# Performance work log

Hardware: AMD Instinct MI355X
Metric: run time of the kernel (lower is better)

## Reference

```python
import jax, jax.numpy as jnp
import numpy as np

N, E, FI, H, T, FO, B = 20000, 320000, 16, 100, 5, 20, 50
EPS = 1e-5


def _glorot(k, shape, fan_in):
    return jax.random.normal(k, shape, jnp.float32) / np.float32(np.sqrt(fan_in))


def setup_inputs():
    key = jax.random.key(0)
    ks = jax.random.split(key, 16)
    inp = {}
    inp['x'] = jax.random.normal(ks[0], (N, FI), jnp.float32)
    inp['edge_index'] = jax.random.randint(ks[1], (2, E), 0, N, jnp.int32)
    inp['edge_attr'] = jax.random.normal(ks[2], (E, 1), jnp.float32)
    inp['batch'] = jnp.sort(jax.random.randint(ks[3], (N,), 0, B, jnp.int32))
    # PNAConv layer 0: input_dim -> hidden (F_in=FI, F_out=FO per tower)
    inp['e0_w'] = _glorot(ks[4], (1, FI), 1); inp['e0_b'] = jnp.zeros((FI,), jnp.float32)
    inp['pre0_w'] = _glorot(ks[5], (T, 3 * FI, FI), 3 * FI); inp['pre0_b'] = jnp.zeros((T, FI), jnp.float32)
    inp['post0_w'] = _glorot(ks[6], (T, 17 * FI, FO), 17 * FI); inp['post0_b'] = jnp.zeros((T, FO), jnp.float32)
    inp['lin0_w'] = _glorot(ks[7], (H, H), H); inp['lin0_b'] = jnp.zeros((H,), jnp.float32)
    inp['bn0_g'] = jnp.ones((H,), jnp.float32); inp['bn0_b'] = jnp.zeros((H,), jnp.float32)
    # PNAConv layers 1..2 (hidden -> hidden), stacked on leading dim 2
    inp['eL_w'] = _glorot(ks[8], (2, 1, H), 1); inp['eL_b'] = jnp.zeros((2, H), jnp.float32)
    inp['preL_w'] = _glorot(ks[9], (2, T, 3 * H, H), 3 * H); inp['preL_b'] = jnp.zeros((2, T, H), jnp.float32)
    inp['postL_w'] = _glorot(ks[10], (2, T, 17 * H, FO), 17 * H); inp['postL_b'] = jnp.zeros((2, T, FO), jnp.float32)
    inp['linL_w'] = _glorot(ks[11], (2, H, H), H); inp['linL_b'] = jnp.zeros((2, H), jnp.float32)
    inp['bnL_g'] = jnp.ones((2, H), jnp.float32); inp['bnL_b'] = jnp.zeros((2, H), jnp.float32)
    # head MLP: H -> 50 -> 25 -> 1
    inp['mlp_w1'] = _glorot(ks[12], (H, 50), H); inp['mlp_b1'] = jnp.zeros((50,), jnp.float32)
    inp['mlp_w2'] = _glorot(ks[13], (50, 25), 50); inp['mlp_b2'] = jnp.zeros((25,), jnp.float32)
    inp['mlp_w3'] = _glorot(ks[14], (25, 1), 25); inp['mlp_b3'] = jnp.zeros((1,), jnp.float32)
    return inp


def _batch_norm(x, g, b):
    mu = x.mean(0)
    var = jnp.mean((x - mu) * (x - mu), 0)  # biased var, as BatchNorm1d (training)
    return (x - mu) * jax.lax.rsqrt(var + EPS) * g + b


def _pna_conv(x, src, dst, edge_attr, cnt, d, log_d, avg_log, avg_lin,
              ew, eb, pw, pb, qw, qb, lw, lb):
    # x: [N,f]; pw: [T,3f,f]; qw: [T,(1+16)f,FO]; lw: [H,H]
    n, f = x.shape
    t = pw.shape[0]
    e = edge_attr @ ew + eb  # [E,f] edge encoder (shared across towers)
    w_i, w_j, w_e = pw[:, :f], pw[:, f:2 * f], pw[:, 2 * f:]
    # pre-MLP on cat([x_i, x_j, e]) without materializing the concat
    m = (jnp.einsum('ef,tfg->etg', x[dst], w_i)
         + jnp.einsum('ef,tfg->etg', x[src], w_j)
         + jnp.einsum('ef,tfg->etg', e, w_e)
         + pb[None])  # [E,T,f]
    dn = d[:, None, None]
    msum = jax.ops.segment_sum(m, dst, n)
    mean = msum / dn
    mean_sq = jax.ops.segment_sum(m * m, dst, n) / dn
    std = jnp.sqrt(jax.nn.relu(mean_sq - mean * mean) + EPS)
    has = (cnt > 0)[:, None, None]
    mn = jnp.where(has, jax.ops.segment_min(m, dst, n), 0.0)
    mx = jnp.where(has, jax.ops.segment_max(m, dst, n), 0.0)
    agg = jnp.concatenate([mean, mn, mx, std], axis=-1)  # [N,T,4f]
    # degree scalers: identity, amplification, attenuation, linear
    scal = jnp.stack([jnp.ones_like(d), log_d / avg_log,
                      avg_log / log_d, d / avg_lin], 0)  # [4,N]
    w_x = qw[:, :f]  # [T,f,FO] block acting on skip features x
    w_s = qw[:, f:].reshape(t, 4, 4 * f, -1).transpose(1, 0, 2, 3)  # [4,T,4f,FO]
    h = (jnp.einsum('nf,tfg->ntg', x, w_x)
         + jnp.einsum('sn,ntf,stfg->ntg', scal, agg, w_s)
         + qb[None])  # [N,T,FO]
    return h.reshape(n, -1) @ lw + lb  # [N,H]


def _model(x, edge_attr, e0_w, e0_b, pre0_w, pre0_b, post0_w, post0_b,
           lin0_w, lin0_b, bn0_g, bn0_b, eL_w, eL_b, preL_w, preL_b,
           postL_w, postL_b, linL_w, linL_b, bnL_g, bnL_b,
           mlp_w1, mlp_b1, mlp_w2, mlp_b2, mlp_w3, mlp_b3,
           edge_index, batch):
    src, dst = edge_index[0], edge_index[1]
    cnt = jax.ops.segment_sum(jnp.ones((E,), x.dtype), dst, N)
    d = jnp.maximum(cnt, 1.0)
    log_d = jnp.log(d + 1.0)
    avg_lin = jnp.mean(cnt)                 # PNA avg_deg['lin']
    avg_log = jnp.mean(jnp.log(cnt + 1.0))  # PNA avg_deg['log']
    h = _pna_conv(x, src, dst, edge_attr, cnt, d, log_d, avg_log, avg_lin,
                  e0_w, e0_b, pre0_w, pre0_b, post0_w, post0_b, lin0_w, lin0_b)
    h = jax.nn.relu(_batch_norm(h, bn0_g, bn0_b))
    for i in range(2):  # zip(convs, batch_norms) -> only num_conv_layers blocks run
        h = _pna_conv(h, src, dst, edge_attr, cnt, d, log_d, avg_log, avg_lin,
                      eL_w[i], eL_b[i], preL_w[i], preL_b[i],
                      postL_w[i], postL_b[i], linL_w[i], linL_b[i])
        h = jax.nn.relu(_batch_norm(h, bnL_g[i], bnL_b[i]))
    # global mean pool over graphs
    gsum = jax.ops.segment_sum(h, batch, B)
    gcnt = jnp.maximum(jax.ops.segment_sum(jnp.ones((N,), h.dtype), batch, B), 1.0)
    g = gsum / gcnt[:, None]
    g = jax.nn.relu(g @ mlp_w1 + mlp_b1)
    g = jax.nn.relu(g @ mlp_w2 + mlp_b2)
    return g @ mlp_w3 + mlp_b3  # [B,1]


def reference(x, edge_attr, e0_w, e0_b, pre0_w, pre0_b, post0_w, post0_b,
              lin0_w, lin0_b, bn0_g, bn0_b, eL_w, eL_b, preL_w, preL_b,
              postL_w, postL_b, linL_w, linL_b, bnL_g, bnL_b,
              mlp_w1, mlp_b1, mlp_w2, mlp_b2, mlp_w3, mlp_b3,
              edge_index, batch):
    return _model(x, edge_attr, e0_w, e0_b, pre0_w, pre0_b, post0_w, post0_b,
                  lin0_w, lin0_b, bn0_g, bn0_b, eL_w, eL_b, preL_w, preL_b,
                  postL_w, postL_b, linL_w, linL_b, bnL_g, bnL_b,
                  mlp_w1, mlp_b1, mlp_w2, mlp_b2, mlp_w3, mlp_b3,
                  edge_index, batch)
```

## Files before the change

kernel.cpp:

```cpp
#include <hip/hip_runtime.h>
#include <hip/hip_bf16.h>
#include <cstddef>

#define N_  20000
#define E_  320000
#define FI_ 16
#define H_  100
#define T_  5
#define FO_ 20
#define B_  50
#define EPSF 1e-5f
#define PR_  200

typedef __attribute__((ext_vector_type(8))) short short8;
typedef __attribute__((ext_vector_type(4))) float f32x4;

static __device__ __forceinline__ unsigned short f2bf(float x) {
  unsigned int u = __builtin_bit_cast(unsigned int, x);
  unsigned int r = (u + 0x7FFFu + ((u >> 16) & 1u)) >> 16;
  return (unsigned short)r;
}
static __device__ __forceinline__ unsigned int packbf(float a, float b) {
  return (unsigned int)f2bf(a) | ((unsigned int)f2bf(b) << 16);
}
static __device__ __forceinline__ float bf2f_lo(unsigned int u) {
  return __builtin_bit_cast(float, (u & 0xFFFFu) << 16);
}
static __device__ __forceinline__ float bf2f_hi(unsigned int u) {
  return __builtin_bit_cast(float, u & 0xFFFF0000u);
}

__global__ void k_count(const int* __restrict__ dst, int* __restrict__ cnt) {
  int e = blockIdx.x * blockDim.x + threadIdx.x;
  if (e < E_) atomicAdd(&cnt[dst[e]], 1);
}

__global__ __launch_bounds__(1024) void k_scan(const int* __restrict__ cnt, int* __restrict__ rowptr) {
  __shared__ int ls[1024];
  const int tid = threadIdx.x;
  const int base = tid * 20;
  int loc[20];
  int lsum = 0;
  #pragma unroll
  for (int i = 0; i < 20; ++i) {
    int idx = base + i;
    int v = (idx < N_) ? cnt[idx] : 0;
    loc[i] = lsum;
    lsum += v;
  }
  ls[tid] = lsum;
  __syncthreads();
  for (int off = 1; off < 1024; off <<= 1) {
    int t = (tid >= off) ? ls[tid - off] : 0;
    __syncthreads();
    ls[tid] += t;
    __syncthreads();
  }
  const int pre = (tid > 0) ? ls[tid - 1] : 0;
  #pragma unroll
  for (int i = 0; i < 20; ++i) {
    int idx = base + i;
    if (idx < N_) rowptr[idx] = pre + loc[i];
  }
  if (tid == 1023) rowptr[N_] = ls[1023];
}

__global__ void k_fill(const int* __restrict__ src, const int* __restrict__ dst,
                       const float* __restrict__ ea, const int* __restrict__ rowptr,
                       int* __restrict__ cursor, int* __restrict__ srcs,
                       float* __restrict__ eav) {
  int e = blockIdx.x * blockDim.x + threadIdx.x;
  if (e < E_) {
    int v = dst[e];
    int p = atomicAdd(&cursor[v], 1);
    int pos = rowptr[v] + p;
    srcs[pos] = src[e];
    eav[pos]  = ea[e];
  }
}

__global__ void k_sumlog(const int* __restrict__ cnt, float* __restrict__ sumlog) {
  int i = blockIdx.x * blockDim.x + threadIdx.x;
  float v = (i < N_) ? logf((float)cnt[i] + 1.0f) : 0.0f;
  #pragma unroll
  for (int off = 32; off > 0; off >>= 1) v += __shfl_down(v, off);
  __shared__ float red[4];
  if ((threadIdx.x & 63) == 0) red[threadIdx.x >> 6] = v;
  __syncthreads();
  if (threadIdx.x == 0) atomicAdd(sumlog, red[0] + red[1] + red[2] + red[3]);
}

__global__ void k_scal(const int* __restrict__ cnt, const float* __restrict__ sumlog,
                       float* __restrict__ scal) {
  int i = blockIdx.x * blockDim.x + threadIdx.x;
  if (i >= N_) return;
  float c  = (float)cnt[i];
  float d  = fmaxf(c, 1.0f);
  float ld = logf(d + 1.0f);
  float avg_log = sumlog[0] * (1.0f / (float)N_);
  float avg_lin = (float)E_ / (float)N_;
  scal[i*4+0] = 1.0f;
  scal[i*4+1] = ld / avg_log;
  scal[i*4+2] = avg_log / ld;
  scal[i*4+3] = d / avg_lin;
}

__global__ void k_edgevec3(const float* __restrict__ p0w, const float* __restrict__ pLw,
                           const float* __restrict__ p0b, const float* __restrict__ pLb,
                           const float* __restrict__ e0w, const float* __restrict__ eLw,
                           const float* __restrict__ e0b, const float* __restrict__ eLb,
                           float* __restrict__ vec_e3, float* __restrict__ cst_e3) {
  const int l = blockIdx.y;
  const int f = l ? H_ : FI_;
  const int C = T_ * f;
  int c = blockIdx.x * blockDim.x + threadIdx.x;
  if (c >= C) return;
  const float* pw = l ? pLw + (size_t)(l-1)*T_*3*H_*H_ : p0w;
  const float* pb = l ? pLb + (l-1)*T_*H_ : p0b;
  const float* ew = l ? eLw + (l-1)*H_ : e0w;
  const float* eb = l ? eLb + (l-1)*H_ : e0b;
  int t = c / f, g = c - t*f;
  const float* wp = pw + (size_t)t*3*f*f + (size_t)2*f*f + g;
  float v = 0.f, s = 0.f;
  for (int ff = 0; ff < f; ++ff) { float wv = wp[(size_t)ff*f]; v += ew[ff]*wv; s += eb[ff]*wv; }
  vec_e3[l*512 + c] = v;
  cst_e3[l*512 + c] = s + pb[c];
}

__global__ void k_pack_preT3(const float* __restrict__ p0w, const float* __restrict__ pLw,
                             unsigned short* __restrict__ Bb3) {
  const int l = blockIdx.y;
  const int f = l ? H_ : FI_;
  const int C = T_ * f;
  const int KPk = l ? 128 : 32;
  const int NcPad = l ? 1024 : 256;
  const int tot = NcPad * KPk;
  int idx = blockIdx.x * blockDim.x + threadIdx.x;
  if (idx >= tot) return;
  const float* pw = l ? pLw + (size_t)(l-1)*T_*3*H_*H_ : p0w;
  int k = idx % KPk, c = idx / KPk;
  float v = 0.f;
  if (c < 2*C && k < f) {
    int half = c / C, cc = c - half*C;
    int t = cc / f, g = cc - t*f;
    v = pw[(size_t)t*3*f*f + (size_t)(half*f + k)*f + g];
  }
  Bb3[(size_t)l*131072 + idx] = f2bf(v);
}

__global__ void k_pack_w23(const float* __restrict__ q0w, const float* __restrict__ qLw,
                           unsigned short* __restrict__ W23) {
  const int l = blockIdx.y;
  const int f = l ? H_ : FI_;
  const int KP = l ? 512 : 96;
  const int tot = T_ * 80 * KP;
  int idx = blockIdx.x * blockDim.x + threadIdx.x;
  if (idx >= tot) return;
  const float* qw = l ? qLw + (size_t)(l-1)*T_*17*H_*FO_ : q0w;
  int k = idx % KP;
  int r = idx / KP;
  int j = r % 80;
  int t = r / 80;
  int s = j / 20, g = j - s*20;
  float v = 0.f;
  if (k < 4*f)                 v = qw[((size_t)t*17*f + f + (size_t)s*4*f + k) * FO_ + g];
  else if (k < 5*f && s == 0)  v = qw[((size_t)t*17*f + (k - 4*f)) * FO_ + g];
  W23[(size_t)l*204800 + idx] = f2bf(v);
}

__global__ void k_pack_lin3(const float* __restrict__ l0w, const float* __restrict__ lLw,
                            unsigned short* __restrict__ Lb3) {
  const int l = blockIdx.y;
  int idx = blockIdx.x * blockDim.x + threadIdx.x;
  if (idx >= 128*128) return;
  const float* lw = l ? lLw + (size_t)(l-1)*H_*H_ : l0w;
  int k = idx & 127, j = idx >> 7;
  float v = (j < H_ && k < H_) ? lw[(size_t)k*H_ + j] : 0.f;
  Lb3[(size_t)l*16384 + idx] = f2bf(v);
}

__global__ __launch_bounds__(256) void k_mmsplit(
    const float* __restrict__ A, const unsigned short* __restrict__ Bb,
    unsigned short* __restrict__ XIb, unsigned short* __restrict__ XJb,
    int M, int K, int KPk, int split)
{
  const int m0 = blockIdx.x * 128;
  const int bn = blockIdx.y * 128;
  const int Nc = 2 * split;
  const int tid = threadIdx.x;
  const int w = tid >> 6, lane = tid & 63;
  const int rl = lane & 15, kq = lane >> 4;
  __shared__ __align__(16) unsigned short As[128*40];
  __shared__ __align__(16) unsigned short Bs[128*40];
  f32x4 acc[2][8];
  #pragma unroll
  for (int mf = 0; mf < 2; ++mf)
    #pragma unroll
    for (int nf = 0; nf < 8; ++nf) acc[mf][nf] = (f32x4){0.f,0.f,0.f,0.f};

  for (int k0 = 0; k0 < KPk; k0 += 32) {
    __syncthreads();
    #pragma unroll
    for (int p = 0; p < 2; ++p) {
      int idx = tid + p*256;
      int row = idx >> 2, q = idx & 3;
      int gm = m0 + row;
      int gk = k0 + q*8;
      unsigned int d0 = 0, d1 = 0, d2 = 0, d3 = 0;
      if (gm < M) {
        if (gk + 8 <= K) {
          const float4 v0 = *(const float4*)&A[(size_t)gm*K + gk];
          const float4 v1 = *(const float4*)&A[(size_t)gm*K + gk + 4];
          d0 = packbf(v0.x, v0.y); d1 = packbf(v0.z, v0.w);
          d2 = packbf(v1.x, v1.y); d3 = packbf(v1.z, v1.w);
        } else if (gk < K) {
          float tmp[8];
          #pragma unroll
          for (int e = 0; e < 8; ++e) tmp[e] = (gk + e < K) ? A[(size_t)gm*K + gk + e] : 0.f;
          d0 = packbf(tmp[0], tmp[1]); d1 = packbf(tmp[2], tmp[3]);
          d2 = packbf(tmp[4], tmp[5]); d3 = packbf(tmp[6], tmp[7]);
        }
      }
      uint4 dv = {d0, d1, d2, d3};
      *(uint4*)&As[row*40 + q*8] = dv;
    }
    #pragma unroll
    for (int p = 0; p < 2; ++p) {
      int idx = tid + p*256;
      int j = idx >> 2, q = idx & 3;
      uint4 v = *(const uint4*)&Bb[((size_t)(bn + j))*KPk + k0 + q*8];
      *(uint4*)&Bs[j*40 + q*8] = v;
    }
    __syncthreads();
    short8 af[2], bf[8];
    #pragma unroll
    for (int mf = 0; mf < 2; ++mf)
      af[mf] = *(const short8*)&As[(w*32 + mf*16 + rl)*40 + kq*8];
    #pragma unroll
    for (int nf = 0; nf < 8; ++nf)
      bf[nf] = *(const short8*)&Bs[(nf*16 + rl)*40 + kq*8];
    #pragma unroll
    for (int mf = 0; mf < 2; ++mf)
      #pragma unroll
      for (int nf = 0; nf < 8; ++nf)
        acc[mf][nf] = __builtin_amdgcn_mfma_f32_16x16x32_bf16(af[mf], bf[nf], acc[mf][nf], 0, 0, 0);
  }
  #pragma unroll
  for (int mf = 0; mf < 2; ++mf)
    #pragma unroll
    for (int nf = 0; nf < 8; ++nf)
      #pragma unroll
      for (int r = 0; r < 4; ++r) {
        int gm = m0 + w*32 + mf*16 + kq*4 + r;
        int gn = bn + nf*16 + rl;
        if (gm < M && gn < Nc) {
          unsigned short v = f2bf(acc[mf][nf][r]);
          if (gn < split) XIb[(size_t)gm*split + gn] = v;
          else            XJb[(size_t)gm*split + (gn - split)] = v;
        }
      }
}

__global__ __launch_bounds__(256) void k_lin(
    const float* __restrict__ A, const unsigned short* __restrict__ Bb,
    const float* __restrict__ bias, float* __restrict__ Cm, int M)
{
  const int m0 = blockIdx.x * 64;
  const int tid = threadIdx.x;
  const int w = tid >> 6, lane = tid & 63;
  const int rl = lane & 15, kq = lane >> 4;
  __shared__ __align__(16) unsigned short As[64*40];
  __shared__ __align__(16) unsigned short Bs[128*40];
  f32x4 acc[8];
  #pragma unroll
  for (int nf = 0; nf < 8; ++nf) acc[nf] = (f32x4){0.f,0.f,0.f,0.f};
  for (int k0 = 0; k0 < 128; k0 += 32) {
    __syncthreads();
    {
      int row = tid >> 2, q = tid & 3;
      int gm = m0 + row;
      int gk = k0 + q*8;
      unsigned int d0=0,d1=0,d2=0,d3=0;
      if (gm < M && gk < H_) {
        if (gk + 8 <= H_) {
          const float4 v0 = *(const float4*)&A[(size_t)gm*H_ + gk];
          const float4 v1 = *(const float4*)&A[(size_t)gm*H_ + gk + 4];
          d0 = packbf(v0.x,v0.y); d1 = packbf(v0.z,v0.w);
          d2 = packbf(v1.x,v1.y); d3 = packbf(v1.z,v1.w);
        } else {
          float tmp[8];
          #pragma unroll
          for (int e = 0; e < 8; ++e) tmp[e] = (gk+e < H_) ? A[(size_t)gm*H_ + gk + e] : 0.f;
          d0 = packbf(tmp[0],tmp[1]); d1 = packbf(tmp[2],tmp[3]);
          d2 = packbf(tmp[4],tmp[5]); d3 = packbf(tmp[6],tmp[7]);
        }
      }
      uint4 dv = {d0,d1,d2,d3};
      *(uint4*)&As[row*40 + q*8] = dv;
    }
    #pragma unroll
    for (int p = 0; p < 2; ++p) {
      int idx = tid + p*256;
      int j = idx >> 2, q = idx & 3;
      uint4 v = *(const uint4*)&Bb[(size_t)j*128 + k0 + q*8];
      *(uint4*)&Bs[j*40 + q*8] = v;
    }
    __syncthreads();
    short8 af = *(const short8*)&As[(w*16 + rl)*40 + kq*8];
    #pragma unroll
    for (int nf = 0; nf < 8; ++nf) {
      short8 bf = *(const short8*)&Bs[(nf*16 + rl)*40 + kq*8];
      acc[nf] = __builtin_amdgcn_mfma_f32_16x16x32_bf16(af, bf, acc[nf], 0, 0, 0);
    }
  }
  #pragma unroll
  for (int nf = 0; nf < 8; ++nf)
    #pragma unroll
    for (int r = 0; r < 4; ++r) {
      int gm = m0 + w*16 + kq*4 + r;
      int gn = nf*16 + rl;
      if (gm < M && gn < H_)
        Cm[(size_t)gm*H_ + gn] = acc[nf][r] + bias[gn];
    }
}

template<int BT>
__global__ __launch_bounds__(BT) void k_agg(
    const unsigned short* __restrict__ XIb, const unsigned short* __restrict__ XJb,
    const int* __restrict__ rowptr, const int* __restrict__ srcs,
    const float* __restrict__ eav, const float* __restrict__ vec_e,
    const float* __restrict__ cst_e, const float* __restrict__ xin,
    unsigned short* __restrict__ Apost, int f, int C, int KP)
{
  __shared__ float vsh[512];
  const int tid = threadIdx.x;
  for (int c = tid; c < C; c += BT) vsh[c] = vec_e[c];
  __syncthreads();
  const int v = blockIdx.x;
  const int start = rowptr[v], end = rowptr[v+1];
  const int half = C >> 1;
  const bool act = (tid < half);
  const float v0 = act ? vsh[tid*2]   : 0.f;
  const float v1 = act ? vsh[tid*2+1] : 0.f;
  const unsigned int* xj = (const unsigned int*)XJb;
  float s10 = 0.f, s11 = 0.f, s20 = 0.f, s21 = 0.f;
  float mn0 = 1e30f, mn1 = 1e30f, mx0 = -1e30f, mx1 = -1e30f;

  int p = start;
  for (; p + 8 <= end; p += 8) {
    int ss[8]; float aa[8];
    #pragma unroll
    for (int q = 0; q < 8; ++q) { ss[q] = srcs[p+q]; aa[q] = eav[p+q]; }
    if (act) {
      unsigned int uu[8];
      #pragma unroll
      for (int q = 0; q < 8; ++q) uu[q] = xj[(size_t)ss[q]*half + tid];
      #pragma unroll
      for (int q = 0; q < 8; ++q) {
        float y0 = fmaf(aa[q], v0, bf2f_lo(uu[q]));
        float y1 = fmaf(aa[q], v1, bf2f_hi(uu[q]));
        s10 += y0; s20 = fmaf(y0,y0,s20); mn0 = fminf(mn0,y0); mx0 = fmaxf(mx0,y0);
        s11 += y1; s21 = fmaf(y1,y1,s21); mn1 = fminf(mn1,y1); mx1 = fmaxf(mx1,y1);
      }
    }
  }
  for (; p < end; ++p) {
    int s = srcs[p];
    float a = eav[p];
    if (act) {
      unsigned int u = xj[(size_t)s*half + tid];
      float y0 = fmaf(a, v0, bf2f_lo(u));
      float y1 = fmaf(a, v1, bf2f_hi(u));
      s10 += y0; s20 = fmaf(y0, y0, s20);
      s11 += y1; s21 = fmaf(y1, y1, s21);
      mn0 = fminf(mn0, y0); mx0 = fmaxf(mx0, y0);
      mn1 = fminf(mn1, y1); mx1 = fmaxf(mx1, y1);
    }
  }

  const int dcnt = end - start;
  if (act) {
    int c0 = tid*2;
    int t = c0 / f, ff = c0 - t*f;
    unsigned int ub = ((const unsigned int*)XIb)[(size_t)v*half + tid];
    float base0 = bf2f_lo(ub) + cst_e[c0];
    float base1 = bf2f_hi(ub) + cst_e[c0 + 1];
    float me0, sd0, lo0, hi0, me1, sd1, lo1, hi1;
    if (dcnt > 0) {
      float inv = 1.0f / (float)dcnt;
      float m10 = s10 * inv, m11 = s11 * inv;
      me0 = base0 + m10; me1 = base1 + m11;
      sd0 = sqrtf(fmaxf(s20*inv - m10*m10, 0.f) + EPSF);
      sd1 = sqrtf(fmaxf(s21*inv - m11*m11, 0.f) + EPSF);
      lo0 = base0 + mn0; hi0 = base0 + mx0;
      lo1 = base1 + mn1; hi1 = base1 + mx1;
    } else {
      me0 = me1 = lo0 = lo1 = hi0 = hi1 = 0.f;
      sd0 = sd1 = sqrtf(EPSF);
    }
    unsigned int* od = (unsigned int*)(Apost + ((size_t)v * T_ + t) * KP);
    int fd = ff >> 1, f2 = f >> 1;
    od[fd]          = packbf(me0, me1);
    od[f2 + fd]     = packbf(lo0, lo1);
    od[2*f2 + fd]   = packbf(hi0, hi1);
    od[3*f2 + fd]   = packbf(sd0, sd1);
  }
  const int rem = KP - 4*f;
  for (int idx = tid; idx < T_*rem; idx += BT) {
    int t = idx / rem, kk = idx - t*rem;
    int k = 4*f + kk;
    unsigned short val = 0;
    if (k < 5*f) val = f2bf(xin[(size_t)v*f + (k - 4*f)]);
    Apost[((size_t)v * T_ + t) * KP + k] = val;
  }
}

__global__ __launch_bounds__(256) void k_postmm(
    const unsigned short* __restrict__ Apost, const unsigned short* __restrict__ W2,
    const float* __restrict__ scal, const float* __restrict__ qb,
    float* __restrict__ h, int KP)
{
  const int t    = blockIdx.y;
  const int m0   = blockIdx.x * 128;
  const int tid  = threadIdx.x;
  const int w    = tid >> 6;
  const int lane = tid & 63;
  const int rl   = lane & 15;
  const int kq   = lane >> 4;
  __shared__ __align__(16) unsigned char smem[128*84*4];
  unsigned short* As = (unsigned short*)smem;
  unsigned short* Bs = As + 128*40;
  f32x4 acc[2][5];
  #pragma unroll
  for (int mf = 0; mf < 2; ++mf)
    #pragma unroll
    for (int nf = 0; nf < 5; ++nf) acc[mf][nf] = (f32x4){0.f,0.f,0.f,0.f};

  const unsigned short* wt = W2 + (size_t)t * 80 * KP;

  for (int k0 = 0; k0 < KP; k0 += 32) {
    __syncthreads();
    #pragma unroll
    for (int p = 0; p < 2; ++p) {
      int idx = tid + p*256;
      int row = idx >> 2, q = idx & 3;
      int gm = m0 + row;
      uint4 v = {0u,0u,0u,0u};
      if (gm < N_) v = *(const uint4*)&Apost[((size_t)gm*T_ + t)*KP + k0 + q*8];
      *(uint4*)&As[row*40 + q*8] = v;
    }
    #pragma unroll
    for (int p = 0; p < 2; ++p) {
      int idx = tid + p*256;
      if (idx < 320) {
        int j = idx >> 2, q = idx & 3;
        uint4 v = *(const uint4*)&wt[(size_t)j*KP + k0 + q*8];
        *(uint4*)&Bs[j*40 + q*8] = v;
      }
    }
    __syncthreads();
    short8 af[2], bf[5];
    #pragma unroll
    for (int mf = 0; mf < 2; ++mf)
      af[mf] = *(const short8*)&As[(w*32 + mf*16 + rl)*40 + kq*8];
    #pragma unroll
    for (int nf = 0; nf < 5; ++nf)
      bf[nf] = *(const short8*)&Bs[(nf*16 + rl)*40 + kq*8];
    #pragma unroll
    for (int mf = 0; mf < 2; ++mf)
      #pragma unroll
      for (int nf = 0; nf < 5; ++nf)
        acc[mf][nf] = __builtin_amdgcn_mfma_f32_16x16x32_bf16(af[mf], bf[nf], acc[mf][nf], 0, 0, 0);
  }
  __syncthreads();
  float (*Pl)[84] = (float (*)[84])smem;
  #pragma unroll
  for (int mf = 0; mf < 2; ++mf)
    #pragma unroll
    for (int nf = 0; nf < 5; ++nf)
      #pragma unroll
      for (int r = 0; r < 4; ++r)
        Pl[w*32 + mf*16 + kq*4 + r][nf*16 + rl] = acc[mf][nf][r];
  __syncthreads();
  for (int idx = tid; idx < 128*FO_; idx += 256) {
    int row = idx / FO_, g = idx - row*FO_;
    int n = m0 + row;
    if (n < N_) {
      const float* p = Pl[row];
      float4 sc = *(const float4*)&scal[n*4];
      h[(size_t)n*(T_*FO_) + t*FO_ + g] =
        p[g] + sc.y*p[20+g] + sc.z*p[40+g] + sc.w*p[60+g] + qb[t*FO_+g];
    }
  }
}

__global__ __launch_bounds__(256) void k_bnsum(const float* __restrict__ h2, float* __restrict__ bnsum) {
  const int tid  = threadIdx.x;
  const int c    = tid & 127;
  const int half = tid >> 7;
  if (c >= H_) return;
  float s = 0.f, s2 = 0.f;
  for (int r = blockIdx.x * 2 + half; r < N_; r += 256) {
    float v = h2[(size_t)r * H_ + c];
    s += v; s2 = fmaf(v, v, s2);
  }
  atomicAdd(&bnsum[c], s);
  atomicAdd(&bnsum[H_ + c], s2);
}

__global__ void k_bnapply(const float* __restrict__ h2, const float* __restrict__ bnsum,
                          const float* __restrict__ gam, const float* __restrict__ bet,
                          float* __restrict__ out) {
  size_t i = (size_t)blockIdx.x * blockDim.x + threadIdx.x;
  if (i >= (size_t)N_*H_) return;
  int c = (int)(i % H_);
  const float invn = 1.0f / (float)N_;
  float mu  = bnsum[c] * invn;
  float var = bnsum[H_ + c] * invn - mu*mu;
  float y = (h2[i] - mu) * rsqrtf(var + EPSF) * gam[c] + bet[c];
  out[i] = fmaxf(y, 0.f);
}

__global__ __launch_bounds__(256) void k_pool(const float* __restrict__ xc, const int* __restrict__ batch,
                                              float* __restrict__ gsum, int* __restrict__ gcnt) {
  __shared__ float Pl[B_][H_];
  __shared__ int cl[B_];
  const int tid = threadIdx.x;
  for (int i = tid; i < B_*H_; i += 256) Pl[i / H_][i % H_] = 0.f;
  for (int i = tid; i < B_; i += 256) cl[i] = 0;
  __syncthreads();
  const int r0 = blockIdx.x * PR_;
  const int rend = (r0 + PR_ < N_) ? r0 + PR_ : N_;
  for (int rr = tid; rr < rend - r0; rr += 256) atomicAdd(&cl[batch[r0 + rr]], 1);
  const int nel = (rend - r0) * H_;
  for (int idx = tid; idx < nel; idx += 256) {
    int rr = idx / H_, c = idx - rr*H_;
    int n = r0 + rr;
    atomicAdd(&Pl[batch[n]][c], xc[(size_t)n*H_ + c]);
  }
  __syncthreads();
  const int blo = batch[r0], bhi = batch[rend-1];
  const int nb = (bhi - blo + 1) * H_;
  for (int idx = tid; idx < nb; idx += 256) {
    int b = blo + idx / H_, c = idx % H_;
    atomicAdd(&gsum[(size_t)b*H_ + c], Pl[b][c]);
  }
  for (int b = blo + tid; b <= bhi; b += 256) atomicAdd(&gcnt[b], cl[b]);
}

__global__ __launch_bounds__(512) void k_mlp(
    const float* __restrict__ gsum, const int* __restrict__ gcnt,
    const float* __restrict__ w1, const float* __restrict__ b1,
    const float* __restrict__ w2, const float* __restrict__ b2,
    const float* __restrict__ w3, const float* __restrict__ b3,
    float* __restrict__ out)
{
  __shared__ float G[B_][H_];
  __shared__ float A1[B_][50];
  __shared__ float A2[B_][25];
  const int tid = threadIdx.x;
  for (int i = tid; i < B_*H_; i += 512) {
    int r = i / H_;
    G[r][i - r*H_] = gsum[i] / fmaxf((float)gcnt[r], 1.0f);
  }
  __syncthreads();
  for (int i = tid; i < B_*50; i += 512) {
    int r = i / 50, c = i - r*50;
    float a = b1[c];
    for (int k = 0; k < H_; ++k) a = fmaf(G[r][k], w1[k*50 + c], a);
    A1[r][c] = fmaxf(a, 0.f);
  }
  __syncthreads();
  for (int i = tid; i < B_*25; i += 512) {
    int r = i / 25, c = i - r*25;
    float a = b2[c];
    for (int k = 0; k < 50; ++k) a = fmaf(A1[r][k], w2[k*25 + c], a);
    A2[r][c] = fmaxf(a, 0.f);
  }
  __syncthreads();
  for (int i = tid; i < B_; i += 512) {
    float a = b3[0];
    for (int k = 0; k < 25; ++k) a = fmaf(A2[i][k], w3[k], a);
    out[i] = a;
  }
}

extern "C" void kernel_launch(void* const* d_in, const int* in_sizes, int n_in,
                              void* d_out, int out_size, void* d_ws, size_t ws_size,
                              hipStream_t stream)
{
  (void)in_sizes; (void)n_in; (void)out_size;
  const float* x0   = (const float*)d_in[0];
  const int*   eidx = (const int*)  d_in[1];
  const float* ea   = (const float*)d_in[2];
  const int*   batch= (const int*)  d_in[3];
  const float* e0w  = (const float*)d_in[4];
  const float* e0b  = (const float*)d_in[5];
  const float* p0w  = (const float*)d_in[6];
  const float* p0b  = (const float*)d_in[7];
  const float* q0w  = (const float*)d_in[8];
  const float* q0b  = (const float*)d_in[9];
  const float* l0w  = (const float*)d_in[10];
  const float* l0b  = (const float*)d_in[11];
  const float* g0   = (const float*)d_in[12];
  const float* b0   = (const float*)d_in[13];
  const float* eLw  = (const float*)d_in[14];
  const float* eLb  = (const float*)d_in[15];
  const float* pLw  = (const float*)d_in[16];
  const float* pLb  = (const float*)d_in[17];
  const float* qLw  = (const float*)d_in[18];
  const float* qLb  = (const float*)d_in[19];
  const float* lLw  = (const float*)d_in[20];
  const float* lLb  = (const float*)d_in[21];
  const float* gL   = (const float*)d_in[22];
  const float* bL   = (const float*)d_in[23];
  const float* w1   = (const float*)d_in[24];
  const float* b1   = (const float*)d_in[25];
  const float* w2   = (const float*)d_in[26];
  const float* b2   = (const float*)d_in[27];
  const float* w3   = (const float*)d_in[28];
  const float* b3   = (const float*)d_in[29];

  const int* src = eidx;
  const int* dst = eidx + E_;

  char* w = (char*)d_ws;
  size_t off = 0;
  auto take = [&](size_t bytes) -> void* {
    void* p = (void*)(w + off);
    off = (off + bytes + 255) & ~(size_t)255;
    return p;
  };
  int*   cnt    = (int*)  take((size_t)N_*4);
  int*   rowptr = (int*)  take((size_t)(N_+1)*4);
  int*   cursor = (int*)  take((size_t)N_*4);
  int*   srcs   = (int*)  take((size_t)E_*4);
  float* eav    = (float*)take((size_t)E_*4);
  float* scal   = (float*)take((size_t)N_*16);
  float* sumlog = (float*)take(256);
  float* bnsum3 = (float*)take((size_t)3*256*4);
  float* vec_e3 = (float*)take((size_t)3*512*4);
  float* cst_e3 = (float*)take((size_t)3*512*4);
  unsigned short* BpreT3 = (unsigned short*)take((size_t)3*131072*2);
  unsigned short* W23    = (unsigned short*)take((size_t)3*204800*2);
  unsigned short* LwT3   = (unsigned short*)take((size_t)3*16384*2);
  unsigned short* XIb    = (unsigned short*)take((size_t)N_*T_*H_*2);
  unsigned short* XJb    = (unsigned short*)take((size_t)N_*T_*H_*2);
  unsigned short* Apost  = (unsigned short*)take((size_t)N_*T_*512*2);
  float* hbuf   = (float*)take((size_t)N_*H_*4);
  float* h2buf  = (float*)take((size_t)N_*H_*4);
  float* xcur   = (float*)take((size_t)N_*H_*4);
  float* gsum   = (float*)take((size_t)B_*H_*4);
  int*   gcnt   = (int*)  take((size_t)B_*4);
  if (off > ws_size) return;

  hipMemsetAsync(cnt,    0, (size_t)N_*4, stream);
  hipMemsetAsync(cursor, 0, (size_t)N_*4, stream);
  hipMemsetAsync(sumlog, 0, 4, stream);
  hipMemsetAsync(bnsum3, 0, (size_t)3*256*4, stream);
  hipMemsetAsync(gsum,   0, (size_t)B_*H_*4, stream);
  hipMemsetAsync(gcnt,   0, (size_t)B_*4, stream);

  k_edgevec3 <<<dim3(2, 3),   dim3(256), 0, stream>>>(p0w, pLw, p0b, pLb, e0w, eLw, e0b, eLb, vec_e3, cst_e3);
  k_pack_preT3<<<dim3(512, 3), dim3(256), 0, stream>>>(p0w, pLw, BpreT3);
  k_pack_w23 <<<dim3(800, 3), dim3(256), 0, stream>>>(q0w, qLw, W23);
  k_pack_lin3<<<dim3(64, 3),  dim3(256), 0, stream>>>(l0w, lLw, LwT3);

  k_count <<<dim3((E_+255)/256), dim3(256), 0, stream>>>(dst, cnt);
  k_scan  <<<dim3(1),            dim3(1024),0, stream>>>(cnt, rowptr);
  k_fill  <<<dim3((E_+255)/256), dim3(256), 0, stream>>>(src, dst, ea, rowptr, cursor, srcs, eav);
  k_sumlog<<<dim3((N_+255)/256), dim3(256), 0, stream>>>(cnt, sumlog);
  k_scal  <<<dim3((N_+255)/256), dim3(256), 0, stream>>>(cnt, sumlog, scal);

  auto layer = [&](int l, const float* xin, int f,
                   const float* qb, const float* lb, const float* bg, const float* bb) {
    const int C   = T_ * f;
    const int KP  = ((5*f + 31) / 32) * 32;
    const int KPk = ((f + 31) / 32) * 32;
    const int gN  = (2*C + 127) / 128;
    const float* vec_e = vec_e3 + l*512;
    const float* cst_e = cst_e3 + l*512;
    const unsigned short* BpreT = BpreT3 + (size_t)l*131072;
    const unsigned short* W2    = W23    + (size_t)l*204800;
    const unsigned short* LwT   = LwT3   + (size_t)l*16384;
    float* bnsum = bnsum3 + l*256;
    k_mmsplit<<<dim3((N_+127)/128, gN), dim3(256), 0, stream>>>(xin, BpreT, XIb, XJb, N_, f, KPk, C);
    if (f == FI_)
      k_agg<64><<<dim3(N_), dim3(64), 0, stream>>>(XIb, XJb, rowptr, srcs, eav, vec_e, cst_e, xin, Apost, f, C, KP);
    else
      k_agg<256><<<dim3(N_), dim3(256), 0, stream>>>(XIb, XJb, rowptr, srcs, eav, vec_e, cst_e, xin, Apost, f, C, KP);
    k_postmm<<<dim3((N_+127)/128, T_), dim3(256), 0, stream>>>(Apost, W2, scal, qb, hbuf, KP);
    k_lin<<<dim3((N_+63)/64), dim3(256), 0, stream>>>(hbuf, LwT, lb, h2buf, N_);
    k_bnsum<<<dim3(128), dim3(256), 0, stream>>>(h2buf, bnsum);
    k_bnapply<<<dim3((unsigned)(((size_t)N_*H_+255)/256)), dim3(256), 0, stream>>>(h2buf, bnsum, bg, bb, xcur);
  };

  layer(0, x0,   FI_, q0b, l0b, g0, b0);
  layer(1, xcur, H_,  qLb, lLb, gL, bL);
  layer(2, xcur, H_,  qLb + T_*FO_, lLb + H_, gL + H_, bL + H_);

  k_pool<<<dim3((N_+PR_-1)/PR_), dim3(256), 0, stream>>>(xcur, batch, gsum, gcnt);
  k_mlp <<<dim3(1), dim3(512), 0, stream>>>(gsum, gcnt, w1, b1, w2, b2, w3, b3, (float*)d_out);
}
```

Baseline: 760.3 us.

## Fuse BN statistics into linear GEMM and feed bf16 activations to GEMM

Folds the batch-norm sum and sum-of-squares reduction into the epilogue of the linear GEMM, using shuffles, shared memory and atomics, which removes the separate k_bnsum pass over the hidden buffer. BN-apply now also writes a padded bf16 copy of the activations (stride 104), and the next layer's pre-GEMM and aggregation read it directly instead of converting fp32 on each load. The aggregation loop is rewritten with 2-wide float vectors to encourage packed math. In exchange there is an extra bf16 write per layer, an extra memset and conversion kernel, and many more atomics on the BN sums.

Result: faster. 703.8 us (-7.4%).

```diff
diff --git a/kernel.cpp b/kernel.cpp
--- a/kernel.cpp
+++ b/kernel.cpp
@@ -14,6 +14,7 @@
 
 typedef __attribute__((ext_vector_type(8))) short short8;
 typedef __attribute__((ext_vector_type(4))) float f32x4;
+typedef __attribute__((ext_vector_type(2))) float f32x2;
 
 static __device__ __forceinline__ unsigned short f2bf(float x) {
   unsigned int u = __builtin_bit_cast(unsigned int, x);
@@ -103,6 +104,12 @@
   scal[i*4+1] = ld / avg_log;
   scal[i*4+2] = avg_log / ld;
   scal[i*4+3] = d / avg_lin;
+}
+
+__global__ void k_cvtx(const float* __restrict__ x0, unsigned int* __restrict__ x0b) {
+  int i = blockIdx.x * blockDim.x + threadIdx.x;
+  if (i >= N_*FI_/2) return;
+  x0b[i] = packbf(x0[2*i], x0[2*i+1]);
 }
 
 __global__ void k_edgevec3(const float* __restrict__ p0w, const float* __restrict__ pLw,
@@ -180,9 +187,9 @@
 }
 
 __global__ __launch_bounds__(256) void k_mmsplit(
-    const float* __restrict__ A, const unsigned short* __restrict__ Bb,
+    const unsigned short* __restrict__ Ab, const unsigned short* __restrict__ Bb,
     unsigned short* __restrict__ XIb, unsigned short* __restrict__ XJb,
-    int M, int K, int KPk, int split)
+    int M, int KA, int KPk, int split)
 {
   const int m0 = blockIdx.x * 128;
   const int bn = blockIdx.y * 128;
@@ -206,23 +213,9 @@
       int row = idx >> 2, q = idx & 3;
       int gm = m0 + row;
       int gk = k0 + q*8;
-      unsigned int d0 = 0, d1 = 0, d2 = 0, d3 = 0;
-      if (gm < M) {
-        if (gk + 8 <= K) {
-          const float4 v0 = *(const float4*)&A[(size_t)gm*K + gk];
-          const float4 v1 = *(const float4*)&A[(size_t)gm*K + gk + 4];
-          d0 = packbf(v0.x, v0.y); d1 = packbf(v0.z, v0.w);
-          d2 = packbf(v1.x, v1.y); d3 = packbf(v1.z, v1.w);
-        } else if (gk < K) {
-          float tmp[8];
-          #pragma unroll
-          for (int e = 0; e < 8; ++e) tmp[e] = (gk + e < K) ? A[(size_t)gm*K + gk + e] : 0.f;
-          d0 = packbf(tmp[0], tmp[1]); d1 = packbf(tmp[2], tmp[3]);
-          d2 = packbf(tmp[4], tmp[5]); d3 = packbf(tmp[6], tmp[7]);
-        }
-      }
-      uint4 dv = {d0, d1, d2, d3};
-      *(uint4*)&As[row*40 + q*8] = dv;
+      uint4 v = {0u,0u,0u,0u};
+      if (gm < M && gk + 8 <= KA) v = *(const uint4*)&Ab[(size_t)gm*KA + gk];
+      *(uint4*)&As[row*40 + q*8] = v;
     }
     #pragma unroll
     for (int p = 0; p < 2; ++p) {
@@ -261,9 +254,10 @@
       }
 }
 
-__global__ __launch_bounds__(256) void k_lin(
+__global__ __launch_bounds__(256) void k_linbn(
     const float* __restrict__ A, const unsigned short* __restrict__ Bb,
-    const float* __restrict__ bias, float* __restrict__ Cm, int M)
+    const float* __restrict__ bias, float* __restrict__ Cm,
+    float* __restrict__ bnsum, int M)
 {
   const int m0 = blockIdx.x * 64;
   const int tid = threadIdx.x;
@@ -271,6 +265,8 @@
   const int rl = lane & 15, kq = lane >> 4;
   __shared__ __align__(16) unsigned short As[64*40];
   __shared__ __align__(16) unsigned short Bs[128*40];
+  __shared__ float bns[4][128];
+  __shared__ float bnq[4][128];
   f32x4 acc[8];
   #pragma unroll
   for (int nf = 0; nf < 8; ++nf) acc[nf] = (f32x4){0.f,0.f,0.f,0.f};
@@ -314,14 +310,29 @@
     }
   }
   #pragma unroll
-  for (int nf = 0; nf < 8; ++nf)
+  for (int nf = 0; nf < 8; ++nf) {
+    int gn = nf*16 + rl;
+    float cs = 0.f, cq = 0.f;
     #pragma unroll
     for (int r = 0; r < 4; ++r) {
       int gm = m0 + w*16 + kq*4 + r;
-      int gn = nf*16 + rl;
-      if (gm < M && gn < H_)
-        Cm[(size_t)gm*H_ + gn] = acc[nf][r] + bias[gn];
-    }
+      if (gm < M && gn < H_) {
+        float v = acc[nf][r] + bias[gn];
+        Cm[(size_t)gm*H_ + gn] = v;
+        cs += v; cq = fmaf(v, v, cq);
+      }
+    }
+    cs += __shfl_xor(cs, 16); cs += __shfl_xor(cs, 32);
+    cq += __shfl_xor(cq, 16); cq += __shfl_xor(cq, 32);
+    if (kq == 0) { bns[w][gn] = cs; bnq[w][gn] = cq; }
+  }
+  __syncthreads();
+  if (tid < H_) {
+    float s = bns[0][tid] + bns[1][tid] + bns[2][tid] + bns[3][tid];
+    float q = bnq[0][tid] + bnq[1][tid] + bnq[2][tid] + bnq[3][tid];
+    atomicAdd(&bnsum[tid], s);
+    atomicAdd(&bnsum[H_ + tid], q);
+  }
 }
 
 template<int BT>
@@ -329,8 +340,8 @@
     const unsigned short* __restrict__ XIb, const unsigned short* __restrict__ XJb,
     const int* __restrict__ rowptr, const int* __restrict__ srcs,
     const float* __restrict__ eav, const float* __restrict__ vec_e,
-    const float* __restrict__ cst_e, const float* __restrict__ xin,
-    unsigned short* __restrict__ Apost, int f, int C, int KP)
+    const float* __restrict__ cst_e, const unsigned short* __restrict__ xb,
+    unsigned short* __restrict__ Apost, int f, int C, int KP, int KA)
 {
   __shared__ float vsh[512];
   const int tid = threadIdx.x;
@@ -340,11 +351,10 @@
   const int start = rowptr[v], end = rowptr[v+1];
   const int half = C >> 1;
   const bool act = (tid < half);
-  const float v0 = act ? vsh[tid*2]   : 0.f;
-  const float v1 = act ? vsh[tid*2+1] : 0.f;
+  f32x2 vv = {act ? vsh[tid*2] : 0.f, act ? vsh[tid*2+1] : 0.f};
   const unsigned int* xj = (const unsigned int*)XJb;
-  float s10 = 0.f, s11 = 0.f, s20 = 0.f, s21 = 0.f;
-  float mn0 = 1e30f, mn1 = 1e30f, mx0 = -1e30f, mx1 = -1e30f;
+  f32x2 s1 = {0.f, 0.f}, s2 = {0.f, 0.f};
+  f32x2 mn = {1e30f, 1e30f}, mx = {-1e30f, -1e30f};
 
   int p = start;
   for (; p + 8 <= end; p += 8) {
@@ -357,10 +367,13 @@
       for (int q = 0; q < 8; ++q) uu[q] = xj[(size_t)ss[q]*half + tid];
       #pragma unroll
       for (int q = 0; q < 8; ++q) {
-        float y0 = fmaf(aa[q], v0, bf2f_lo(uu[q]));
-        float y1 = fmaf(aa[q], v1, bf2f_hi(uu[q]));
-        s10 += y0; s20 = fmaf(y0,y0,s20); mn0 = fminf(mn0,y0); mx0 = fmaxf(mx0,y0);
-        s11 += y1; s21 = fmaf(y1,y1,s21); mn1 = fminf(mn1,y1); mx1 = fmaxf(mx1,y1);
+        f32x2 u2 = {bf2f_lo(uu[q]), bf2f_hi(uu[q])};
+        f32x2 a2 = {aa[q], aa[q]};
+        f32x2 y = __builtin_elementwise_fma(a2, vv, u2);
+        s1 += y;
+        s2 = __builtin_elementwise_fma(y, y, s2);
+        mn = __builtin_elementwise_min(mn, y);
+        mx = __builtin_elementwise_max(mx, y);
       }
     }
   }
@@ -369,12 +382,13 @@
     float a = eav[p];
     if (act) {
       unsigned int u = xj[(size_t)s*half + tid];
-      float y0 = fmaf(a, v0, bf2f_lo(u));
-      float y1 = fmaf(a, v1, bf2f_hi(u));
-      s10 += y0; s20 = fmaf(y0, y0, s20);
-      s11 += y1; s21 = fmaf(y1, y1, s21);
-      mn0 = fminf(mn0, y0); mx0 = fmaxf(mx0, y0);
-      mn1 = fminf(mn1, y1); mx1 = fmaxf(mx1, y1);
+      f32x2 u2 = {bf2f_lo(u), bf2f_hi(u)};
+      f32x2 a2 = {a, a};
+      f32x2 y = __builtin_elementwise_fma(a2, vv, u2);
+      s1 += y;
+      s2 = __builtin_elementwise_fma(y, y, s2);
+      mn = __builtin_elementwise_min(mn, y);
+      mx = __builtin_elementwise_max(mx, y);
     }
   }
 
@@ -388,12 +402,12 @@
     float me0, sd0, lo0, hi0, me1, sd1, lo1, hi1;
     if (dcnt > 0) {
       float inv = 1.0f / (float)dcnt;
-      float m10 = s10 * inv, m11 = s11 * inv;
+      float m10 = s1.x * inv, m11 = s1.y * inv;
       me0 = base0 + m10; me1 = base1 + m11;
-      sd0 = sqrtf(fmaxf(s20*inv - m10*m10, 0.f) + EPSF);
-      sd1 = sqrtf(fmaxf(s21*inv - m11*m11, 0.f) + EPSF);
-      lo0 = base0 + mn0; hi0 = base0 + mx0;
-      lo1 = base1 + mn1; hi1 = base1 + mx1;
+      sd0 = sqrtf(fmaxf(s2.x*inv - m10*m10, 0.f) + EPSF);
+      sd1 = sqrtf(fmaxf(s2.y*inv - m11*m11, 0.f) + EPSF);
+      lo0 = base0 + mn.x; hi0 = base0 + mx.x;
+      lo1 = base1 + mn.y; hi1 = base1 + mx.y;
     } else {
       me0 = me1 = lo0 = lo1 = hi0 = hi1 = 0.f;
       sd0 = sd1 = sqrtf(EPSF);
@@ -410,7 +424,7 @@
     int t = idx / rem, kk = idx - t*rem;
     int k = 4*f + kk;
     unsigned short val = 0;
-    if (k < 5*f) val = f2bf(xin[(size_t)v*f + (k - 4*f)]);
+    if (k < 5*f) val = xb[(size_t)v*KA + (k - 4*f)];
     Apost[((size_t)v * T_ + t) * KP + k] = val;
   }
 }
@@ -494,31 +508,20 @@
   }
 }
 
-__global__ __launch_bounds__(256) void k_bnsum(const float* __restrict__ h2, float* __restrict__ bnsum) {
-  const int tid  = threadIdx.x;
-  const int c    = tid & 127;
-  const int half = tid >> 7;
-  if (c >= H_) return;
-  float s = 0.f, s2 = 0.f;
-  for (int r = blockIdx.x * 2 + half; r < N_; r += 256) {
-    float v = h2[(size_t)r * H_ + c];
-    s += v; s2 = fmaf(v, v, s2);
-  }
-  atomicAdd(&bnsum[c], s);
-  atomicAdd(&bnsum[H_ + c], s2);
-}
-
 __global__ void k_bnapply(const float* __restrict__ h2, const float* __restrict__ bnsum,
                           const float* __restrict__ gam, const float* __restrict__ bet,
-                          float* __restrict__ out) {
+                          float* __restrict__ out, unsigned short* __restrict__ outb) {
   size_t i = (size_t)blockIdx.x * blockDim.x + threadIdx.x;
   if (i >= (size_t)N_*H_) return;
   int c = (int)(i % H_);
+  int n = (int)(i / H_);
   const float invn = 1.0f / (float)N_;
   float mu  = bnsum[c] * invn;
   float var = bnsum[H_ + c] * invn - mu*mu;
   float y = (h2[i] - mu) * rsqrtf(var + EPSF) * gam[c] + bet[c];
-  out[i] = fmaxf(y, 0.f);
+  y = fmaxf(y, 0.f);
+  out[i] = y;
+  outb[(size_t)n*104 + c] = f2bf(y);
 }
 
 __global__ __launch_bounds__(256) void k_pool(const float* __restrict__ xc, const int* __restrict__ batch,
@@ -644,6 +647,8 @@
   unsigned short* BpreT3 = (unsigned short*)take((size_t)3*131072*2);
   unsigned short* W23    = (unsigned short*)take((size_t)3*204800*2);
   unsigned short* LwT3   = (unsigned short*)take((size_t)3*16384*2);
+  unsigned short* x0b    = (unsigned short*)take((size_t)N_*FI_*2);
+  unsigned short* xcurb  = (unsigned short*)take((size_t)N_*104*2);
   unsigned short* XIb    = (unsigned short*)take((size_t)N_*T_*H_*2);
   unsigned short* XJb    = (unsigned short*)take((size_t)N_*T_*H_*2);
   unsigned short* Apost  = (unsigned short*)take((size_t)N_*T_*512*2);
@@ -658,6 +663,7 @@
   hipMemsetAsync(cursor, 0, (size_t)N_*4, stream);
   hipMemsetAsync(sumlog, 0, 4, stream);
   hipMemsetAsync(bnsum3, 0, (size_t)3*256*4, stream);
+  hipMemsetAsync(xcurb,  0, (size_t)N_*104*2, stream);
   hipMemsetAsync(gsum,   0, (size_t)B_*H_*4, stream);
   hipMemsetAsync(gcnt,   0, (size_t)B_*4, stream);
 
@@ -665,6 +671,7 @@
   k_pack_preT3<<<dim3(512, 3), dim3(256), 0, stream>>>(p0w, pLw, BpreT3);
   k_pack_w23 <<<dim3(800, 3), dim3(256), 0, stream>>>(q0w, qLw, W23);
   k_pack_lin3<<<dim3(64, 3),  dim3(256), 0, stream>>>(l0w, lLw, LwT3);
+  k_cvtx     <<<dim3((N_*FI_/2+255)/256), dim3(256), 0, stream>>>(x0, (unsigned int*)x0b);
 
   k_count <<<dim3((E_+255)/256), dim3(256), 0, stream>>>(dst, cnt);
   k_scan  <<<dim3(1),            dim3(1024),0, stream>>>(cnt, rowptr);
@@ -672,7 +679,7 @@
   k_sumlog<<<dim3((N_+255)/256), dim3(256), 0, stream>>>(cnt, sumlog);
   k_scal  <<<dim3((N_+255)/256), dim3(256), 0, stream>>>(cnt, sumlog, scal);
 
-  auto layer = [&](int l, const float* xin, int f,
+  auto layer = [&](int l, const unsigned short* xb, int f, int KA,
                    const float* qb, const float* lb, const float* bg, const float* bb) {
     const int C   = T_ * f;
     const int KP  = ((5*f + 31) / 32) * 32;
@@ -684,20 +691,19 @@
     const unsigned short* W2    = W23    + (size_t)l*204800;
     const unsigned short* LwT   = LwT3   + (size_t)l*16384;
     float* bnsum = bnsum3 + l*256;
-    k_mmsplit<<<dim3((N_+127)/128, gN), dim3(256), 0, stream>>>(xin, BpreT, XIb, XJb, N_, f, KPk, C);
+    k_mmsplit<<<dim3((N_+127)/128, gN), dim3(256), 0, stream>>>(xb, BpreT, XIb, XJb, N_, KA, KPk, C);
     if (f == FI_)
-      k_agg<64><<<dim3(N_), dim3(64), 0, stream>>>(XIb, XJb, rowptr, srcs, eav, vec_e, cst_e, xin, Apost, f, C, KP);
+      k_agg<64><<<dim3(N_), dim3(64), 0, stream>>>(XIb, XJb, rowptr, srcs, eav, vec_e, cst_e, xb, Apost, f, C, KP, KA);
     else
-      k_agg<256><<<dim3(N_), dim3(256), 0, stream>>>(XIb, XJb, rowptr, srcs, eav, vec_e, cst_e, xin, Apost, f, C, KP);
+      k_agg<256><<<dim3(N_), dim3(256), 0, stream>>>(XIb, XJb, rowptr, srcs, eav, vec_e, cst_e, xb, Apost, f, C, KP, KA);
     k_postmm<<<dim3((N_+127)/128, T_), dim3(256), 0, stream>>>(Apost, W2, scal, qb, hbuf, KP);
-    k_lin<<<dim3((N_+63)/64), dim3(256), 0, stream>>>(hbuf, LwT, lb, h2buf, N_);
-    k_bnsum<<<dim3(128), dim3(256), 0, stream>>>(h2buf, bnsum);
-    k_bnapply<<<dim3((unsigned)(((size_t)N_*H_+255)/256)), dim3(256), 0, stream>>>(h2buf, bnsum, bg, bb, xcur);
+    k_linbn<<<dim3((N_+63)/64), dim3(256), 0, stream>>>(hbuf, LwT, lb, h2buf, bnsum, N_);
+    k_bnapply<<<dim3((unsigned)(((size_t)N_*H_+255)/256)), dim3(256), 0, stream>>>(h2buf, bnsum, bg, bb, xcur, xcurb);
   };
 
-  layer(0, x0,   FI_, q0b, l0b, g0, b0);
-  layer(1, xcur, H_,  qLb, lLb, gL, bL);
-  layer(2, xcur, H_,  qLb + T_*FO_, lLb + H_, gL + H_, bL + H_);
+  layer(0, x0b,   FI_, 16,  q0b, l0b, g0, b0);
+  layer(1, xcurb, H_,  104, qLb, lLb, gL, bL);
+  layer(2, xcurb, H_,  104, qLb + T_*FO_, lLb + H_, gL + H_, bL + H_);
 
   k_pool<<<dim3((N_+PR_-1)/PR_), dim3(256), 0, stream>>>(xcur, batch, gsum, gcnt);
   k_mlp <<<dim3(1), dim3(512), 0, stream>>>(gsum, gcnt, w1, b1, w2, b2, w3, b3, (float*)d_out);
```
